# Performance work log

Measured on AMD Instinct MI355X. Metric: run time of the kernel, lower is better.

Reference implementation:

```python
import jax, jax.numpy as jnp
import numpy as np

B, S, D_MODEL = 4, 4096, 2048
D_SPACE = 128
N_C, N_QK, N_V = 512, 512, 512
TOPK_C, TOPK_QK, TOPK_V = 8, 4, 6


def setup_inputs() -> dict:
    key = jax.random.key(0)
    k1, k2, k3, k4 = jax.random.split(key, 4)
    x = jax.random.normal(k1, (B, S, D_MODEL), dtype=jnp.float32)
    importance = jax.random.uniform(k2, (B, S), dtype=jnp.float32)
    proj_w = jax.random.normal(k3, (D_SPACE, D_MODEL), dtype=jnp.float32) * (1.0 / np.sqrt(D_MODEL))
    proj_b = jnp.zeros((D_SPACE,), dtype=jnp.float32)
    neuron_emb = jax.random.normal(k4, (N_C + N_QK + N_V, D_SPACE), dtype=jnp.float32) * 0.02
    return {"x": x, "importance": importance, "proj_w": proj_w, "proj_b": proj_b, "neuron_emb": neuron_emb}


def _topk_sparsify(w, k):
    # torch: topk -> scatter into zeros -> renormalize
    vals, idx = jax.lax.top_k(w, k)                      # [B,k]
    b = jnp.arange(w.shape[0])[:, None]
    sparse = jnp.zeros_like(w).at[b, idx].set(vals)      # [B,n]
    return sparse / (sparse.sum(axis=-1, keepdims=True) + 1e-8)


def reference(x, importance, proj_w, proj_b, neuron_emb):
    # eval mode: dropout off, no starvation bonus, no EMA / aux loss
    h = jnp.einsum("bsd,ed->bse", x, proj_w) + proj_b          # [B,S,d_space]
    nrm = jnp.linalg.norm(neuron_emb, axis=-1, keepdims=True)
    emb_n = neuron_emb / jnp.maximum(nrm, 1e-12)               # F.normalize
    logits = jnp.einsum("bse,ne->bsn", h, emb_n)               # [B,S,total]

    log_c = logits[..., :N_C]
    log_qk = logits[..., N_C:N_C + N_QK]                        # expand_Q == expand_K slice
    log_v = logits[..., N_C + N_QK:]

    pref_c = jax.nn.softmax(log_c, axis=-1)
    pref_qk = jax.nn.softmax(log_qk, axis=-1)
    pref_v = jax.nn.softmax(log_v, axis=-1)

    dense_c = jnp.einsum("bs,bsn->bn", importance, pref_c)
    dense_qk = jnp.einsum("bs,bsn->bn", importance, pref_qk)
    dense_v = jnp.einsum("bs,bsn->bn", importance, pref_v)

    cw = _topk_sparsify(dense_c, TOPK_C)
    qw = _topk_sparsify(dense_qk, TOPK_QK)   # Q and K use identical logits in eval
    kw = _topk_sparsify(dense_qk, TOPK_QK)
    vw = _topk_sparsify(dense_v, TOPK_V)
    return jnp.stack([cw, qw, kw, vw])       # [4, B, 512]
```

## Files before the change

kernel.cpp:

```cpp
#include <hip/hip_runtime.h>
#include <hip/hip_bf16.h>

#define BATCH 4
#define S_TOT 4096
#define ROWS (BATCH * S_TOT)
#define DM 2048
#define DSP 128
#define NSEG 512

typedef short short8 __attribute__((ext_vector_type(8)));
typedef float f32x16 __attribute__((ext_vector_type(16)));

static __device__ inline short f2bf(float v, float& back) {
  unsigned u = __float_as_uint(v);
  unsigned r = u + 0x7FFFu + ((u >> 16) & 1u);
  unsigned short hs = (unsigned short)(r >> 16);
  back = __uint_as_float(((unsigned)hs) << 16);
  return (short)hs;
}


__global__ __launch_bounds__(64) void k0_prep(const float* __restrict__ W,
                                              const float* __restrict__ emb,
                                              short* __restrict__ wHi,
                                              short* __restrict__ wLo,
                                              short* __restrict__ eHi,
                                              short* __restrict__ eLo) {
  const int l = threadIdx.x;
  if (blockIdx.x < 512) {
    const int tc = blockIdx.x;
    const int t = tc >> 7, c = tc & 127;
    const int n = t * 32 + (l & 31);
    const int k = c * 16 + (l >> 5) * 8;
    const float4 a0 = *(const float4*)&W[(size_t)n * DM + k];
    const float4 a1 = *(const float4*)&W[(size_t)n * DM + k + 4];
    const float av[8] = {a0.x, a0.y, a0.z, a0.w, a1.x, a1.y, a1.z, a1.w};
    short8 hi8, lo8; float bk;
    #pragma unroll
    for (int e = 0; e < 8; ++e) {
      hi8[e] = f2bf(av[e], bk); lo8[e] = f2bf(av[e] - bk, bk);
    }
    const size_t idx = (size_t)tc * 64 + l;
    ((short8*)wHi)[idx] = hi8;
    ((short8*)wLo)[idx] = lo8;
  } else {
    const int row = blockIdx.x - 512;
    __shared__ short sh[128], sl[128];
    float2 v = *(const float2*)&emb[row * 128 + l * 2];
    float ss = v.x * v.x + v.y * v.y;
    #pragma unroll
    for (int m = 32; m; m >>= 1) ss += __shfl_xor(ss, m);
    const float inv = 1.0f / fmaxf(sqrtf(ss), 1e-12f);
    float bk;
    const float ox = v.x * inv, oy = v.y * inv;
    sh[2 * l] = f2bf(ox, bk);     sl[2 * l] = f2bf(ox - bk, bk);
    sh[2 * l + 1] = f2bf(oy, bk); sl[2 * l + 1] = f2bf(oy - bk, bk);
    __syncthreads();
    if (l < 32) {
      const int split = l >> 4, kc = (l >> 1) & 7, kh = l & 1;
      const short* src = (split ? sl : sh) + kc * 16 + kh * 8;
      const short8 val = *(const short8*)src;
      const size_t idx = (size_t)(row >> 5) * 4096 + kc * 512 +
                         ((row & 31) + 32 * kh) * 8;
      *(short8*)((split ? eLo : eHi) + idx) = val;
    }
  }
}

__global__ __launch_bounds__(512, 4) void k1_fused(const float* __restrict__ x,
                                                   const short* __restrict__ wHi,
                                                   const short* __restrict__ wLo,
                                                   const float* __restrict__ bias,
                                                   short* __restrict__ hHi,
                                                   short* __restrict__ hLo) {
  __shared__ __align__(16) float hs[4][32][132];
  __shared__ float bsh[128];
  const int t = threadIdx.x;
  const int wave = t >> 6, lane = t & 63;
  const int fr = lane & 31, ks = lane >> 5;
  const int m0 = blockIdx.x * 32;

  if (t < 128) bsh[t] = bias[t];

  const float* xp = x + (size_t)(m0 + fr) * DM + wave * 256 + ks * 8;
  const short8* bhp = (const short8*)wHi + (size_t)wave * 16 * 64 + lane;
  const short8* blp = (const short8*)wLo + (size_t)wave * 16 * 64 + lane;

  f32x16 acc[4] = {};

  #pragma unroll
  for (int c = 0; c < 16; ++c) {
    const float4 a0 = *(const float4*)(xp + c * 16);
    const float4 a1 = *(const float4*)(xp + c * 16 + 4);
    const float av[8] = {a0.x, a0.y, a0.z, a0.w, a1.x, a1.y, a1.z, a1.w};
    short8 ah, al; float bk;
    #pragma unroll
    for (int e = 0; e < 8; ++e) {
      ah[e] = f2bf(av[e], bk); al[e] = f2bf(av[e] - bk, bk);
    }
    #pragma unroll
    for (int t2 = 0; t2 < 4; ++t2) {
      const short8 bh = bhp[(size_t)t2 * 8192 + c * 64];
      const short8 bl = blp[(size_t)t2 * 8192 + c * 64];
      acc[t2] = __builtin_amdgcn_mfma_f32_32x32x16_bf16(ah, bh, acc[t2], 0, 0, 0);
      acc[t2] = __builtin_amdgcn_mfma_f32_32x32x16_bf16(ah, bl, acc[t2], 0, 0, 0);
      acc[t2] = __builtin_amdgcn_mfma_f32_32x32x16_bf16(al, bh, acc[t2], 0, 0, 0);
    }
  }

  if (wave < 4) {
    #pragma unroll
    for (int t2 = 0; t2 < 4; ++t2)
      #pragma unroll
      for (int reg = 0; reg < 16; ++reg) {
        const int row = (reg & 3) + 8 * (reg >> 2) + 4 * ks;
        hs[wave][row][t2 * 32 + fr] = acc[t2][reg];
      }
  }
  __syncthreads();
  if (wave >= 4) {
    #pragma unroll
    for (int t2 = 0; t2 < 4; ++t2)
      #pragma unroll
      for (int reg = 0; reg < 16; ++reg) {
        const int row = (reg & 3) + 8 * (reg >> 2) + 4 * ks;
        hs[wave - 4][row][t2 * 32 + fr] += acc[t2][reg];
      }
  }
  __syncthreads();

  {
    const int row = t >> 4, kc8 = t & 15;
    float v[8];
    #pragma unroll
    for (int j = 0; j < 8; ++j) {
      v[j] = ((hs[0][row][kc8 * 8 + j] + hs[1][row][kc8 * 8 + j]) +
              (hs[2][row][kc8 * 8 + j] + hs[3][row][kc8 * 8 + j])) +
             bsh[kc8 * 8 + j];
    }
    short8 hi8, lo8; float bk;
    #pragma unroll
    for (int e = 0; e < 8; ++e) {
      hi8[e] = f2bf(v[e], bk); lo8[e] = f2bf(v[e] - bk, bk);
    }
    const int kc = kc8 >> 1, kh = kc8 & 1;
    const size_t idx = (size_t)blockIdx.x * 512 + kc * 64 + (row + 32 * kh);
    ((short8*)hHi)[idx] = hi8;
    ((short8*)hLo)[idx] = lo8;
  }
}

__global__ __launch_bounds__(512, 2) void k2_mfma(const short* __restrict__ hHi,
                                                  const short* __restrict__ hLo,
                                                  const short* __restrict__ eHi,
                                                  const short* __restrict__ eLo,
                                                  const float* __restrict__ imp,
                                                  float* __restrict__ partials) {
  const int t = threadIdx.x;
  const int m0 = blockIdx.x * 64;
  const int seg = blockIdx.y;
  const int wave = t >> 6, lane = t & 63;
  const int wr = wave >> 2;
  const int wc = wave & 3;
  const int fr = lane & 31;
  const int hi = lane >> 5;

  __shared__ float redA[2][32][4];
  __shared__ float redB[2][32][4];
  __shared__ float ldsD[2][512];

  f32x16 acc[4] = {};

  const short8* pAh = (const short8*)hHi + ((m0 >> 5) + wr) * 512 + lane;
  const short8* pAl = (const short8*)hLo + ((m0 >> 5) + wr) * 512 + lane;
  const short8* pBh = (const short8*)eHi + (seg * 16 + wc * 4) * 512 + lane;
  const short8* pBl = (const short8*)eLo + (seg * 16 + wc * 4) * 512 + lane;

  #pragma unroll
  for (int kc = 0; kc < 8; ++kc) {
    const short8 ah = pAh[kc * 64];
    const short8 al = pAl[kc * 64];
    #pragma unroll
    for (int t2 = 0; t2 < 4; ++t2) {
      const short8 bh = pBh[t2 * 512 + kc * 64];
      const short8 bl = pBl[t2 * 512 + kc * 64];
      acc[t2] = __builtin_amdgcn_mfma_f32_32x32x16_bf16(ah, bh, acc[t2], 0, 0, 0);
      acc[t2] = __builtin_amdgcn_mfma_f32_32x32x16_bf16(ah, bl, acc[t2], 0, 0, 0);
      acc[t2] = __builtin_amdgcn_mfma_f32_32x32x16_bf16(al, bh, acc[t2], 0, 0, 0);
    }
  }

  float mx[16];
  #pragma unroll
  for (int r = 0; r < 16; ++r) {
    float m = fmaxf(fmaxf(acc[0][r], acc[1][r]), fmaxf(acc[2][r], acc[3][r]));
    #pragma unroll
    for (int k = 1; k < 32; k <<= 1) m = fmaxf(m, __shfl_xor(m, k));
    mx[r] = m;
  }
  if (fr == 0) {
    #pragma unroll
    for (int r = 0; r < 16; ++r)
      redA[wr][(r & 3) + 8 * (r >> 2) + 4 * hi][wc] = mx[r];
  }
  __syncthreads();
  float M[16];
  #pragma unroll
  for (int r = 0; r < 16; ++r) {
    const int row = (r & 3) + 8 * (r >> 2) + 4 * hi;
    M[r] = fmaxf(fmaxf(redA[wr][row][0], redA[wr][row][1]),
                 fmaxf(redA[wr][row][2], redA[wr][row][3]));
  }

  float sm[16];
  #pragma unroll
  for (int r = 0; r < 16; ++r) {
    float s = 0.0f;
    #pragma unroll
    for (int t2 = 0; t2 < 4; ++t2) {
      const float p = __expf(acc[t2][r] - M[r]);
      acc[t2][r] = p;
      s += p;
    }
    #pragma unroll
    for (int k = 1; k < 32; k <<= 1) s += __shfl_xor(s, k);
    sm[r] = s;
  }
  if (fr == 0) {
    #pragma unroll
    for (int r = 0; r < 16; ++r)
      redB[wr][(r & 3) + 8 * (r >> 2) + 4 * hi][wc] = sm[r];
  }
  __syncthreads();
  float w[16];
  #pragma unroll
  for (int r = 0; r < 16; ++r) {
    const int row = (r & 3) + 8 * (r >> 2) + 4 * hi;
    const float S = (redB[wr][row][0] + redB[wr][row][1]) +
                    (redB[wr][row][2] + redB[wr][row][3]);
    w[r] = imp[m0 + wr * 32 + row] / S;
  }

  #pragma unroll
  for (int t2 = 0; t2 < 4; ++t2) {
    float d = 0.0f;
    #pragma unroll
    for (int r = 0; r < 16; ++r) d = fmaf(acc[t2][r], w[r], d);
    d += __shfl_xor(d, 32);
    if (hi == 0) ldsD[wr][wc * 128 + t2 * 32 + fr] = d;
  }
  __syncthreads();
  partials[((size_t)seg * 256 + blockIdx.x) * 512 + t] = ldsD[0][t] + ldsD[1][t];
}

__global__ __launch_bounds__(256) void k3_topk(const float* __restrict__ partials,
                                               float* __restrict__ out) {
  const int b = blockIdx.x;
  const int seg = blockIdx.y;
  const int tid = threadIdx.x;
  const int K = (seg == 0) ? 8 : ((seg == 1) ? 4 : 6);

  __shared__ float v[512];
  __shared__ float wv[8];
  __shared__ int wi[8];
  __shared__ float redv[4];
  __shared__ int redi[4];

  const float* src = partials + ((size_t)seg * 256 + b * 64) * 512;
  float a0 = 0.f, a1 = 0.f, a2 = 0.f, a3 = 0.f;
  float b0 = 0.f, b1 = 0.f, b2 = 0.f, b3 = 0.f;
  for (int j = 0; j < 64; j += 4) {
    a0 += src[(size_t)(j + 0) * 512 + tid];
    a1 += src[(size_t)(j + 1) * 512 + tid];
    a2 += src[(size_t)(j + 2) * 512 + tid];
    a3 += src[(size_t)(j + 3) * 512 + tid];
    b0 += src[(size_t)(j + 0) * 512 + tid + 256];
    b1 += src[(size_t)(j + 1) * 512 + tid + 256];
    b2 += src[(size_t)(j + 2) * 512 + tid + 256];
    b3 += src[(size_t)(j + 3) * 512 + tid + 256];
  }
  v[tid] = (a0 + a1) + (a2 + a3);
  v[tid + 256] = (b0 + b1) + (b2 + b3);
  __syncthreads();

  for (int t = 0; t < K; ++t) {
    const float v0 = v[tid], v1 = v[tid + 256];
    float bv; int bi;
    if (v1 > v0) { bv = v1; bi = tid + 256; } else { bv = v0; bi = tid; }
    #pragma unroll
    for (int m = 1; m < 64; m <<= 1) {
      const float ov = __shfl_xor(bv, m);
      const int oi = __shfl_xor(bi, m);
      if (ov > bv || (ov == bv && oi < bi)) { bv = ov; bi = oi; }
    }
    if ((tid & 63) == 0) { redv[tid >> 6] = bv; redi[tid >> 6] = bi; }
    __syncthreads();
    if (tid == 0) {
      float best = redv[0]; int besti = redi[0];
      for (int q = 1; q < 4; ++q)
        if (redv[q] > best || (redv[q] == best && redi[q] < besti)) {
          best = redv[q]; besti = redi[q];
        }
      wv[t] = best; wi[t] = besti;
      v[besti] = -3.0e38f;
    }
    __syncthreads();
  }

  float s = 1e-8f;
  for (int t = 0; t < K; ++t) s += wv[t];

  const int slot0 = (seg == 0) ? 0 : ((seg == 1) ? 1 : 3);
  float* o0 = out + slot0 * (BATCH * NSEG) + b * NSEG;
  o0[tid] = 0.0f; o0[tid + 256] = 0.0f;
  float* o1 = nullptr;
  if (seg == 1) {
    o1 = out + 2 * (BATCH * NSEG) + b * NSEG;
    o1[tid] = 0.0f; o1[tid + 256] = 0.0f;
  }
  __syncthreads();
  if (tid < K) {
    const float val = wv[tid] / s;
    o0[wi[tid]] = val;
    if (seg == 1) o1[wi[tid]] = val;
  }
}

extern "C" void kernel_launch(void* const* d_in, const int* in_sizes, int n_in,
                              void* d_out, int out_size, void* d_ws, size_t ws_size,
                              hipStream_t stream) {
  (void)in_sizes; (void)n_in; (void)out_size; (void)ws_size;
  const float* x    = (const float*)d_in[0];
  const float* imp  = (const float*)d_in[1];
  const float* W    = (const float*)d_in[2];
  const float* bias = (const float*)d_in[3];
  const float* emb  = (const float*)d_in[4];
  float* out = (float*)d_out;

  float* partials = (float*)d_ws;
  short* hHi      = (short*)(partials + 768 * 512);
  short* hLo      = hHi + 2097152;
  short* eHi      = hLo + 2097152;
  short* eLo      = eHi + 196608;
  short* wHi      = eLo + 196608;
  short* wLo      = wHi + 262144;

  k0_prep<<<512 + 1536, 64, 0, stream>>>(W, emb, wHi, wLo, eHi, eLo);
  k1_fused<<<ROWS / 32, 512, 0, stream>>>(x, wHi, wLo, bias, hHi, hLo);
  k2_mfma<<<dim3(ROWS / 64, 3), 512, 0, stream>>>(hHi, hLo, eHi, eLo, imp, partials);
  k3_topk<<<dim3(BATCH, 3), 256, 0, stream>>>(partials, out);
}
```

Baseline: 104.3 us.

## Stage x tiles through LDS with async double-buffered loads and repartition waves

The projection kernel now streams x into a double-buffered, XOR-swizzled LDS tile using global_load_lds, so the next K-step loads while MFMAs run on the current one. Work is split differently across the 8 waves: each wave owns one 32-column output tile and half of each K chunk, instead of one K slice covering all four column tiles. This cuts the cross-wave reduction from four partial buffers to two and gives the accumulator fewer registers. The cost is a block barrier on every K step, plus each wave now reads its share of the W tiles across the whole K range.

```diff
diff --git a/kernel.cpp b/kernel.cpp
--- a/kernel.cpp
+++ b/kernel.cpp
@@ -18,6 +18,11 @@
   back = __uint_as_float(((unsigned)hs) << 16);
   return (short)hs;
 }
+
+#define GLL16(gsrc, ldst)                                                       \
+  __builtin_amdgcn_global_load_lds(                                             \
+      (const __attribute__((address_space(1))) void*)(gsrc),                    \
+      (__attribute__((address_space(3))) void*)(ldst), 16, 0, 0)
 
 
 __global__ __launch_bounds__(64) void k0_prep(const float* __restrict__ W,
@@ -73,59 +78,78 @@
                                                    const float* __restrict__ bias,
                                                    short* __restrict__ hHi,
                                                    short* __restrict__ hLo) {
-  __shared__ __align__(16) float hs[4][32][132];
+  __shared__ __align__(16) float As[2][32][128];
+  __shared__ __align__(16) float hsum[32][132];
   __shared__ float bsh[128];
   const int t = threadIdx.x;
   const int wave = t >> 6, lane = t & 63;
   const int fr = lane & 31, ks = lane >> 5;
+  const int kh = wave >> 2, wc = wave & 3;
   const int m0 = blockIdx.x * 32;
 
   if (t < 128) bsh[t] = bias[t];
 
-  const float* xp = x + (size_t)(m0 + fr) * DM + wave * 256 + ks * 8;
-  const short8* bhp = (const short8*)wHi + (size_t)wave * 16 * 64 + lane;
-  const short8* blp = (const short8*)wLo + (size_t)wave * 16 * 64 + lane;
-
-  f32x16 acc[4] = {};
-
-  #pragma unroll
-  for (int c = 0; c < 16; ++c) {
-    const float4 a0 = *(const float4*)(xp + c * 16);
-    const float4 a1 = *(const float4*)(xp + c * 16 + 4);
-    const float av[8] = {a0.x, a0.y, a0.z, a0.w, a1.x, a1.y, a1.z, a1.w};
-    short8 ah, al; float bk;
-    #pragma unroll
-    for (int e = 0; e < 8; ++e) {
-      ah[e] = f2bf(av[e], bk); al[e] = f2bf(av[e] - bk, bk);
-    }
-    #pragma unroll
-    for (int t2 = 0; t2 < 4; ++t2) {
-      const short8 bh = bhp[(size_t)t2 * 8192 + c * 64];
-      const short8 bl = blp[(size_t)t2 * 8192 + c * 64];
-      acc[t2] = __builtin_amdgcn_mfma_f32_32x32x16_bf16(ah, bh, acc[t2], 0, 0, 0);
-      acc[t2] = __builtin_amdgcn_mfma_f32_32x32x16_bf16(ah, bl, acc[t2], 0, 0, 0);
-      acc[t2] = __builtin_amdgcn_mfma_f32_32x32x16_bf16(al, bh, acc[t2], 0, 0, 0);
-    }
-  }
-
-  if (wave < 4) {
-    #pragma unroll
-    for (int t2 = 0; t2 < 4; ++t2)
+  const int r0 = 4 * wave + ks;
+  const int r1 = r0 + 2;
+  const float* xsrc0 = x + (size_t)(m0 + r0) * DM + ((fr ^ (r0 & 7)) << 2);
+  const float* xsrc1 = x + (size_t)(m0 + r1) * DM + ((fr ^ (r1 & 7)) << 2);
+  float* AsF = &As[0][0][0];
+  float* dst0 = AsF + wave * 512;
+  float* dst1 = dst0 + 256;
+
+  const short8* bhBase = (const short8*)wHi + (size_t)(wc * 128) * 64 + lane;
+  const short8* blBase = (const short8*)wLo + (size_t)(wc * 128) * 64 + lane;
+  const int fr7 = fr & 7;
+
+  f32x16 acc = {};
+
+  GLL16(xsrc0, dst0);
+  GLL16(xsrc1, dst1);
+  __syncthreads();
+
+  #pragma unroll 2
+  for (int step = 0; step < 16; ++step) {
+    const int buf = step & 1;
+    if (step + 1 < 16) {
+      GLL16(xsrc0 + (step + 1) * 128, AsF + (buf ^ 1) * 4096 + wave * 512);
+      GLL16(xsrc1 + (step + 1) * 128, AsF + (buf ^ 1) * 4096 + wave * 512 + 256);
+    }
+    const float* abase = AsF + buf * 4096 + fr * 128;
+    #pragma unroll
+    for (int c = 0; c < 4; ++c) {
+      const int g0 = kh * 16 + c * 4 + ks * 2;
+      const float4 a0 = *(const float4*)(abase + ((g0 ^ fr7) << 2));
+      const float4 a1 = *(const float4*)(abase + (((g0 + 1) ^ fr7) << 2));
+      const float av[8] = {a0.x, a0.y, a0.z, a0.w, a1.x, a1.y, a1.z, a1.w};
+      short8 ah, al; float bk;
       #pragma unroll
-      for (int reg = 0; reg < 16; ++reg) {
-        const int row = (reg & 3) + 8 * (reg >> 2) + 4 * ks;
-        hs[wave][row][t2 * 32 + fr] = acc[t2][reg];
+      for (int e = 0; e < 8; ++e) {
+        ah[e] = f2bf(av[e], bk); al[e] = f2bf(av[e] - bk, bk);
       }
-  }
-  __syncthreads();
-  if (wave >= 4) {
-    #pragma unroll
-    for (int t2 = 0; t2 < 4; ++t2)
-      #pragma unroll
-      for (int reg = 0; reg < 16; ++reg) {
-        const int row = (reg & 3) + 8 * (reg >> 2) + 4 * ks;
-        hs[wave - 4][row][t2 * 32 + fr] += acc[t2][reg];
-      }
+      const int kcg = step * 8 + kh * 4 + c;
+      const short8 bh = bhBase[(size_t)kcg * 64];
+      const short8 bl = blBase[(size_t)kcg * 64];
+      acc = __builtin_amdgcn_mfma_f32_32x32x16_bf16(ah, bh, acc, 0, 0, 0);
+      acc = __builtin_amdgcn_mfma_f32_32x32x16_bf16(ah, bl, acc, 0, 0, 0);
+      acc = __builtin_amdgcn_mfma_f32_32x32x16_bf16(al, bh, acc, 0, 0, 0);
+    }
+    __syncthreads();
+  }
+
+  if (kh == 0) {
+    #pragma unroll
+    for (int reg = 0; reg < 16; ++reg) {
+      const int row = (reg & 3) + 8 * (reg >> 2) + 4 * ks;
+      hsum[row][wc * 32 + fr] = acc[reg];
+    }
+  }
+  __syncthreads();
+  if (kh == 1) {
+    #pragma unroll
+    for (int reg = 0; reg < 16; ++reg) {
+      const int row = (reg & 3) + 8 * (reg >> 2) + 4 * ks;
+      hsum[row][wc * 32 + fr] += acc[reg];
+    }
   }
   __syncthreads();
 
@@ -133,18 +157,15 @@
     const int row = t >> 4, kc8 = t & 15;
     float v[8];
     #pragma unroll
-    for (int j = 0; j < 8; ++j) {
-      v[j] = ((hs[0][row][kc8 * 8 + j] + hs[1][row][kc8 * 8 + j]) +
-              (hs[2][row][kc8 * 8 + j] + hs[3][row][kc8 * 8 + j])) +
-             bsh[kc8 * 8 + j];
-    }
+    for (int j = 0; j < 8; ++j)
+      v[j] = hsum[row][kc8 * 8 + j] + bsh[kc8 * 8 + j];
     short8 hi8, lo8; float bk;
     #pragma unroll
     for (int e = 0; e < 8; ++e) {
       hi8[e] = f2bf(v[e], bk); lo8[e] = f2bf(v[e] - bk, bk);
     }
-    const int kc = kc8 >> 1, kh = kc8 & 1;
-    const size_t idx = (size_t)blockIdx.x * 512 + kc * 64 + (row + 32 * kh);
+    const int kc = kc8 >> 1, kh2 = kc8 & 1;
+    const size_t idx = (size_t)blockIdx.x * 512 + kc * 64 + (row + 32 * kh2);
     ((short8*)hHi)[idx] = hi8;
     ((short8*)hLo)[idx] = lo8;
   }
```

Result: slower. 113.1 us (+8.5%).

## Split projection GEMM over K across two blocks and use hardware bf16 packing

Applied to the files above, without the earlier changes.

The x·W projection kernel now splits the 2048-wide reduction into two halves on a second grid dimension, doubling the number of blocks, and each half writes fp32 partial sums to a new workspace buffer. A new pack kernel adds the two partials plus the bias and performs the hi/lo bf16 split. The manual round-to-nearest conversion is replaced by the v_cvt_pk_bf16_f32 instruction. This is meant to raise parallelism and cut conversion ALU work, at the cost of an extra launch and an additional 16 MB of fp32 partials written and read back.

```diff
diff --git a/kernel.cpp b/kernel.cpp
--- a/kernel.cpp
+++ b/kernel.cpp
@@ -17,6 +17,25 @@
   unsigned short hs = (unsigned short)(r >> 16);
   back = __uint_as_float(((unsigned)hs) << 16);
   return (short)hs;
+}
+
+static __device__ inline unsigned cvtpk2(float a, float b) {
+  unsigned r;
+  asm("v_cvt_pk_bf16_f32 %0, %1, %2" : "=v"(r) : "v"(a), "v"(b));
+  return r;
+}
+static __device__ inline void cvt8(const float* v, short8& hi8, short8& lo8) {
+  union { short8 s; unsigned u[4]; } H, L;
+  #pragma unroll
+  for (int w = 0; w < 4; ++w) {
+    const float f0 = v[2 * w], f1 = v[2 * w + 1];
+    const unsigned u = cvtpk2(f0, f1);
+    const float b0 = __uint_as_float(u << 16);
+    const float b1 = __uint_as_float(u & 0xffff0000u);
+    L.u[w] = cvtpk2(f0 - b0, f1 - b1);
+    H.u[w] = u;
+  }
+  hi8 = H.s; lo8 = L.s;
 }
 
 
@@ -67,41 +86,35 @@
   }
 }
 
-__global__ __launch_bounds__(512, 4) void k1_fused(const float* __restrict__ x,
-                                                   const short* __restrict__ wHi,
-                                                   const short* __restrict__ wLo,
-                                                   const float* __restrict__ bias,
-                                                   short* __restrict__ hHi,
-                                                   short* __restrict__ hLo) {
+__global__ __launch_bounds__(512, 2) void k1_mfma(const float* __restrict__ x,
+                                                  const short* __restrict__ wHi,
+                                                  const short* __restrict__ wLo,
+                                                  float* __restrict__ hPart) {
   __shared__ __align__(16) float hs[4][32][132];
-  __shared__ float bsh[128];
   const int t = threadIdx.x;
   const int wave = t >> 6, lane = t & 63;
   const int fr = lane & 31, ks = lane >> 5;
   const int m0 = blockIdx.x * 32;
-
-  if (t < 128) bsh[t] = bias[t];
-
-  const float* xp = x + (size_t)(m0 + fr) * DM + wave * 256 + ks * 8;
-  const short8* bhp = (const short8*)wHi + (size_t)wave * 16 * 64 + lane;
-  const short8* blp = (const short8*)wLo + (size_t)wave * 16 * 64 + lane;
+  const int y  = blockIdx.y;
+
+  const float* xb = x + (size_t)(m0 + fr) * DM + y * 1024 + wave * 128 + ks * 8;
+  const int kcb = y * 64 + wave * 8;
+  const short8* pBh = (const short8*)wHi + (size_t)kcb * 64 + lane;
+  const short8* pBl = (const short8*)wLo + (size_t)kcb * 64 + lane;
 
   f32x16 acc[4] = {};
 
   #pragma unroll
-  for (int c = 0; c < 16; ++c) {
-    const float4 a0 = *(const float4*)(xp + c * 16);
-    const float4 a1 = *(const float4*)(xp + c * 16 + 4);
+  for (int kc = 0; kc < 8; ++kc) {
+    const float4 a0 = *(const float4*)(xb + kc * 16);
+    const float4 a1 = *(const float4*)(xb + kc * 16 + 4);
     const float av[8] = {a0.x, a0.y, a0.z, a0.w, a1.x, a1.y, a1.z, a1.w};
-    short8 ah, al; float bk;
-    #pragma unroll
-    for (int e = 0; e < 8; ++e) {
-      ah[e] = f2bf(av[e], bk); al[e] = f2bf(av[e] - bk, bk);
-    }
+    short8 ah, al;
+    cvt8(av, ah, al);
     #pragma unroll
     for (int t2 = 0; t2 < 4; ++t2) {
-      const short8 bh = bhp[(size_t)t2 * 8192 + c * 64];
-      const short8 bl = blp[(size_t)t2 * 8192 + c * 64];
+      const short8 bh = pBh[(size_t)t2 * 8192 + kc * 64];
+      const short8 bl = pBl[(size_t)t2 * 8192 + kc * 64];
       acc[t2] = __builtin_amdgcn_mfma_f32_32x32x16_bf16(ah, bh, acc[t2], 0, 0, 0);
       acc[t2] = __builtin_amdgcn_mfma_f32_32x32x16_bf16(ah, bl, acc[t2], 0, 0, 0);
       acc[t2] = __builtin_amdgcn_mfma_f32_32x32x16_bf16(al, bh, acc[t2], 0, 0, 0);
@@ -128,26 +141,41 @@
       }
   }
   __syncthreads();
-
   {
     const int row = t >> 4, kc8 = t & 15;
     float v[8];
     #pragma unroll
-    for (int j = 0; j < 8; ++j) {
-      v[j] = ((hs[0][row][kc8 * 8 + j] + hs[1][row][kc8 * 8 + j]) +
-              (hs[2][row][kc8 * 8 + j] + hs[3][row][kc8 * 8 + j])) +
-             bsh[kc8 * 8 + j];
-    }
-    short8 hi8, lo8; float bk;
-    #pragma unroll
-    for (int e = 0; e < 8; ++e) {
-      hi8[e] = f2bf(v[e], bk); lo8[e] = f2bf(v[e] - bk, bk);
-    }
-    const int kc = kc8 >> 1, kh = kc8 & 1;
-    const size_t idx = (size_t)blockIdx.x * 512 + kc * 64 + (row + 32 * kh);
-    ((short8*)hHi)[idx] = hi8;
-    ((short8*)hLo)[idx] = lo8;
-  }
+    for (int j = 0; j < 8; ++j)
+      v[j] = (hs[0][row][kc8 * 8 + j] + hs[1][row][kc8 * 8 + j]) +
+             (hs[2][row][kc8 * 8 + j] + hs[3][row][kc8 * 8 + j]);
+    float* hp = hPart + (size_t)y * ROWS * DSP + (size_t)(m0 + row) * DSP + kc8 * 8;
+    *(float4*)hp = make_float4(v[0], v[1], v[2], v[3]);
+    *(float4*)(hp + 4) = make_float4(v[4], v[5], v[6], v[7]);
+  }
+}
+
+__global__ __launch_bounds__(256) void k1c_pack(const float* __restrict__ hPart,
+                                                const float* __restrict__ bias,
+                                                short* __restrict__ hHi,
+                                                short* __restrict__ hLo) {
+  const int gid = blockIdx.x * 256 + threadIdx.x;
+  const int row = gid >> 4, kc8 = gid & 15;
+  const float* p0 = hPart + (size_t)row * 128 + kc8 * 8;
+  const float* p1 = p0 + (size_t)ROWS * 128;
+  const float4 a0 = *(const float4*)p0, a1 = *(const float4*)(p0 + 4);
+  const float4 b0 = *(const float4*)p1, b1 = *(const float4*)(p1 + 4);
+  const float4 c0 = *(const float4*)&bias[kc8 * 8];
+  const float4 c1 = *(const float4*)&bias[kc8 * 8 + 4];
+  const float v[8] = {a0.x + b0.x + c0.x, a0.y + b0.y + c0.y,
+                      a0.z + b0.z + c0.z, a0.w + b0.w + c0.w,
+                      a1.x + b1.x + c1.x, a1.y + b1.y + c1.y,
+                      a1.z + b1.z + c1.z, a1.w + b1.w + c1.w};
+  short8 hi8, lo8;
+  cvt8(v, hi8, lo8);
+  const int kc = kc8 >> 1, kh = kc8 & 1;
+  const size_t idx = (size_t)(row >> 5) * 512 + kc * 64 + ((row & 31) + 32 * kh);
+  ((short8*)hHi)[idx] = hi8;
+  ((short8*)hLo)[idx] = lo8;
 }
 
 __global__ __launch_bounds__(512, 2) void k2_mfma(const short* __restrict__ hHi,
@@ -338,15 +366,17 @@
   float* out = (float*)d_out;
 
   float* partials = (float*)d_ws;
-  short* hHi      = (short*)(partials + 768 * 512);
+  short* hHi      = (short*)(partials + 393216);
   short* hLo      = hHi + 2097152;
   short* eHi      = hLo + 2097152;
   short* eLo      = eHi + 196608;
   short* wHi      = eLo + 196608;
   short* wLo      = wHi + 262144;
+  float* hPart    = (float*)(wLo + 262144);
 
   k0_prep<<<512 + 1536, 64, 0, stream>>>(W, emb, wHi, wLo, eHi, eLo);
-  k1_fused<<<ROWS / 32, 512, 0, stream>>>(x, wHi, wLo, bias, hHi, hLo);
+  k1_mfma<<<dim3(ROWS / 32, 2), 512, 0, stream>>>(x, wHi, wLo, hPart);
+  k1c_pack<<<1024, 256, 0, stream>>>(hPart, bias, hHi, hLo);
   k2_mfma<<<dim3(ROWS / 64, 3), 512, 0, stream>>>(hHi, hLo, eHi, eLo, imp, partials);
   k3_topk<<<dim3(BATCH, 3), 256, 0, stream>>>(partials, out);
 }
```

New measurement: 122.3 us. +17.3%, slower.
